# Kernel optimization log

Hardware: AMD Instinct MI355X
Metric: run time of the kernel (lower is better)

Reference implementation:

```python
import jax, jax.numpy as jnp
import numpy as np

C_Z = 128
C_H = 128
EPS = 1e-5


def _layer_norm(x, gamma, beta):
    mu = jnp.mean(x, axis=-1, keepdims=True)
    var = jnp.mean(jnp.square(x - mu), axis=-1, keepdims=True)
    return (x - mu) * jax.lax.rsqrt(var + EPS) * gamma + beta


def setup_inputs() -> dict:
    key = jax.random.key(0)
    ks = jax.random.split(key, 8)
    B, N = 1, 512
    s_z = 1.0 / np.sqrt(C_Z)
    s_h = 1.0 / np.sqrt(C_H)
    return {
        "z": jax.random.normal(ks[0], (B, N, N, C_Z), dtype=jnp.float32),
        "mask": jnp.ones((B, N, N), dtype=jnp.float32),
        # linear_ab_p: c_z -> 2*c_hidden
        "w_ab_p": jax.random.normal(ks[1], (2 * C_H, C_Z), dtype=jnp.float32) * s_z,
        "b_ab_p": jnp.zeros((2 * C_H,), dtype=jnp.float32),
        # linear_ab_g: c_z -> 2*c_hidden (gating init)
        "w_ab_g": jax.random.normal(ks[2], (2 * C_H, C_Z), dtype=jnp.float32) * s_z,
        "b_ab_g": jnp.ones((2 * C_H,), dtype=jnp.float32),
        # linear_g: c_z -> c_z (gating init)
        "w_g": jax.random.normal(ks[3], (C_Z, C_Z), dtype=jnp.float32) * s_z,
        "b_g": jnp.ones((C_Z,), dtype=jnp.float32),
        # linear_z: c_hidden -> c_z (final init)
        "w_z": jax.random.normal(ks[4], (C_Z, C_H), dtype=jnp.float32) * s_h,
        "b_z": jnp.zeros((C_Z,), dtype=jnp.float32),
        # layer norms
        "ln_in_g": jnp.ones((C_Z,), dtype=jnp.float32),
        "ln_in_b": jnp.zeros((C_Z,), dtype=jnp.float32),
        "ln_out_g": jnp.ones((C_H,), dtype=jnp.float32),
        "ln_out_b": jnp.zeros((C_H,), dtype=jnp.float32),
    }


def reference(z, mask, w_ab_p, b_ab_p, w_ab_g, b_ab_g, w_g, b_g, w_z, b_z,
              ln_in_g, ln_in_b, ln_out_g, ln_out_b):
    # [B, N, N, C] pair representation; outgoing triangle update
    zn = _layer_norm(z, ln_in_g, ln_in_b)
    m = mask[..., None]  # [B, N, N, 1]
    # gated dual projections: sigmoid(W_g z) * mask * (W_p z)  -> [B, N, N, 2H]
    gate = jax.nn.sigmoid(jnp.einsum("bijc,hc->bijh", zn, w_ab_g) + b_ab_g) * m
    ab = gate * (jnp.einsum("bijc,hc->bijh", zn, w_ab_p) + b_ab_p)
    a, b = jnp.split(ab, 2, axis=-1)  # each [B, N, N, H]
    # outgoing: x[b,i,j,h] = sum_k a[b,i,k,h] * b[b,j,k,h]
    x = jnp.einsum("bikh,bjkh->bijh", a, b)
    x = _layer_norm(x, ln_out_g, ln_out_b)
    out = (jnp.einsum("bijh,ch->bijc", x, w_z) + b_z)
    g = jax.nn.sigmoid(jnp.einsum("bijc,dc->bijd", zn, w_g) + b_g)
    return out * g
```

## Files before the change

kernel.cpp:

```cpp
#include <hip/hip_runtime.h>
#include <math.h>

#define NN 512
#define RR 262144
#define EPS_F 1e-5f

typedef unsigned short u16;
typedef unsigned int u32;
typedef __bf16 bf16x8 __attribute__((ext_vector_type(8)));
typedef float f32x4 __attribute__((ext_vector_type(4)));

__device__ __forceinline__ u16 f2bs(float f) {
  __bf16 h = (__bf16)f;
  return __builtin_bit_cast(u16, h);
}
__device__ __forceinline__ float bs2f(u16 u) {
  return (float)__builtin_bit_cast(__bf16, u);
}
__device__ __forceinline__ float sigmoidf_(float x) {
  return 1.f / (1.f + __expf(-x));
}

__global__ __launch_bounds__(256) void k_ln_in(const float* __restrict__ z,
                                               const float* __restrict__ g,
                                               const float* __restrict__ b,
                                               u16* __restrict__ zn) {
  const int w = threadIdx.x >> 6, l = threadIdx.x & 63;
  const long r = (long)blockIdx.x * 4 + w;
  const float2 v = *(const float2*)(z + r * 128 + l * 2);
  float s = v.x + v.y, sq = v.x * v.x + v.y * v.y;
#pragma unroll
  for (int m = 1; m < 64; m <<= 1) {
    s += __shfl_xor(s, m);
    sq += __shfl_xor(sq, m);
  }
  const float mu = s * 0.0078125f;
  const float var = sq * 0.0078125f - mu * mu;
  const float rs = rsqrtf(var + EPS_F);
  const float2 gg = *(const float2*)(g + l * 2);
  const float2 bb = *(const float2*)(b + l * 2);
  const u32 o = (u32)f2bs((v.x - mu) * rs * gg.x + bb.x) |
                ((u32)f2bs((v.y - mu) * rs * gg.y + bb.y) << 16);
  *(u32*)(zn + r * 128 + l * 2) = o;
}

__global__ __launch_bounds__(256) void k_proj(
    const u16* __restrict__ zn, const float* __restrict__ mask,
    const float* __restrict__ w_ab_p, const float* __restrict__ b_ab_p,
    const float* __restrict__ w_ab_g, const float* __restrict__ b_ab_g,
    const float* __restrict__ w_g, const float* __restrict__ b_g,
    u16* __restrict__ a_t, u16* __restrict__ b_t, u16* __restrict__ g_out) {
  __shared__ __align__(16) u16 As[128 * 136];
  __shared__ __align__(16) u16 Bs[128 * 136];
  __shared__ float maskS[128];
  const int t = threadIdx.x;
  const int tt = blockIdx.y;
  const long row0 = (long)blockIdx.x * 128;

  {
    const int row = t >> 1, half = t & 1;
    const uint4* src = (const uint4*)(zn + (row0 + row) * 128 + half * 64);
    uint4* dst = (uint4*)(As + row * 136 + half * 64);
#pragma unroll
    for (int i = 0; i < 8; ++i) dst[i] = src[i];
  }
  {
    const int n = t >> 1, half = t & 1;
    const float* src;
    if (tt < 4) {
      const int srow = tt * 64 + ((n >> 5) << 4) + (n & 15);
      src = (((n >> 4) & 1) ? w_ab_g : w_ab_p) + srow * 128 + half * 64;
    } else {
      src = w_g + n * 128 + half * 64;
    }
    u16* dst = Bs + n * 136 + half * 64;
#pragma unroll
    for (int i = 0; i < 16; ++i) {
      const float4 v = *(const float4*)(src + i * 4);
      dst[i * 4 + 0] = f2bs(v.x);
      dst[i * 4 + 1] = f2bs(v.y);
      dst[i * 4 + 2] = f2bs(v.z);
      dst[i * 4 + 3] = f2bs(v.w);
    }
  }
  if (t < 128) maskS[t] = mask[row0 + t];
  __syncthreads();

  const int lane = t & 63, wv = t >> 6;
  const int quad = lane >> 4, tl = lane & 15;
  const int wm = wv >> 1, wn = wv & 1;
  f32x4 acc[4][4];
#pragma unroll
  for (int mt = 0; mt < 4; ++mt)
#pragma unroll
    for (int nt = 0; nt < 4; ++nt) acc[mt][nt] = (f32x4){0.f, 0.f, 0.f, 0.f};

#pragma unroll
  for (int ks = 0; ks < 4; ++ks) {
    bf16x8 af[4], bfr[4];
#pragma unroll
    for (int mt = 0; mt < 4; ++mt)
      af[mt] = *(const bf16x8*)(As + (wm * 64 + mt * 16 + tl) * 136 + ks * 32 + quad * 8);
#pragma unroll
    for (int nt = 0; nt < 4; ++nt)
      bfr[nt] = *(const bf16x8*)(Bs + (wn * 64 + nt * 16 + tl) * 136 + ks * 32 + quad * 8);
#pragma unroll
    for (int mt = 0; mt < 4; ++mt)
#pragma unroll
      for (int nt = 0; nt < 4; ++nt)
        acc[mt][nt] = __builtin_amdgcn_mfma_f32_16x16x32_bf16(af[mt], bfr[nt], acc[mt][nt], 0, 0, 0);
  }

  if (tt < 4) {
    __syncthreads();
    u16* trans = As;
#pragma unroll
    for (int b2 = 0; b2 < 2; ++b2) {
      const int hl = wn * 32 + b2 * 16 + tl;
      const int hg = tt * 64 + hl;
      const float bp = b_ab_p[hg], bg = b_ab_g[hg];
#pragma unroll
      for (int mt = 0; mt < 4; ++mt) {
#pragma unroll
        for (int rg = 0; rg < 4; ++rg) {
          const int r = wm * 64 + mt * 16 + quad * 4 + rg;
          const float p = acc[mt][2 * b2][rg] + bp;
          const float gt = acc[mt][2 * b2 + 1][rg] + bg;
          trans[hl * 136 + r] = f2bs(sigmoidf_(gt) * maskS[r] * p);
        }
      }
    }
    __syncthreads();
    const int hl = t >> 2, qq = t & 3;
    const int hg = tt * 64 + hl;
    u16* dbuf = (tt < 2) ? a_t : b_t;
    const int hb = (tt < 2) ? hg : hg - 128;
    const uint4* src = (const uint4*)(trans + hl * 136 + qq * 32);
    uint4* dst = (uint4*)(dbuf + (long)hb * RR + row0 + qq * 32);
#pragma unroll
    for (int i = 0; i < 4; ++i) dst[i] = src[i];
  } else {
#pragma unroll
    for (int nt = 0; nt < 4; ++nt) {
      const int c = wn * 64 + nt * 16 + tl;
      const float bgc = b_g[c];
#pragma unroll
      for (int mt = 0; mt < 4; ++mt)
#pragma unroll
        for (int rg = 0; rg < 4; ++rg) {
          const int r = wm * 64 + mt * 16 + quad * 4 + rg;
          g_out[(row0 + r) * (long)128 + c] = f2bs(sigmoidf_(acc[mt][nt][rg] + bgc));
        }
    }
  }
}

__global__ __launch_bounds__(256) void k_tri(const u16* __restrict__ a_t,
                                             const u16* __restrict__ b_t,
                                             u16* __restrict__ x_t) {
  __shared__ __align__(16) u16 As[128 * 72];
  __shared__ __align__(16) u16 Bs[128 * 72];
  const int t = threadIdx.x;
  const int h = blockIdx.y;
  const int i0 = (blockIdx.x >> 2) * 128, j0 = (blockIdx.x & 3) * 128;
  const u16* Ag = a_t + (long)h * RR;
  const u16* Bg = b_t + (long)h * RR;
  const int lane = t & 63, wv = t >> 6;
  const int quad = lane >> 4, tl = lane & 15;
  const int wm = wv >> 1, wn = wv & 1;
  const int chunk = t & 7, rb = t >> 3;

  f32x4 acc[4][4];
#pragma unroll
  for (int mt = 0; mt < 4; ++mt)
#pragma unroll
    for (int nt = 0; nt < 4; ++nt) acc[mt][nt] = (f32x4){0.f, 0.f, 0.f, 0.f};

  for (int kt = 0; kt < 8; ++kt) {
    __syncthreads();
#pragma unroll
    for (int p = 0; p < 4; ++p) {
      const int row = rb + p * 32;
      *(uint4*)(As + row * 72 + chunk * 8) =
          *(const uint4*)(Ag + (long)(i0 + row) * 512 + kt * 64 + chunk * 8);
      *(uint4*)(Bs + row * 72 + chunk * 8) =
          *(const uint4*)(Bg + (long)(j0 + row) * 512 + kt * 64 + chunk * 8);
    }
    __syncthreads();
#pragma unroll
    for (int ks = 0; ks < 2; ++ks) {
      bf16x8 af[4], bfr[4];
#pragma unroll
      for (int mt = 0; mt < 4; ++mt)
        af[mt] = *(const bf16x8*)(As + (wm * 64 + mt * 16 + tl) * 72 + ks * 32 + quad * 8);
#pragma unroll
      for (int nt = 0; nt < 4; ++nt)
        bfr[nt] = *(const bf16x8*)(Bs + (wn * 64 + nt * 16 + tl) * 72 + ks * 32 + quad * 8);
#pragma unroll
      for (int mt = 0; mt < 4; ++mt)
#pragma unroll
        for (int nt = 0; nt < 4; ++nt)
          acc[mt][nt] = __builtin_amdgcn_mfma_f32_16x16x32_bf16(af[mt], bfr[nt], acc[mt][nt], 0, 0, 0);
    }
  }
#pragma unroll
  for (int mt = 0; mt < 4; ++mt)
#pragma unroll
    for (int nt = 0; nt < 4; ++nt)
#pragma unroll
      for (int rg = 0; rg < 4; ++rg) {
        const int i = i0 + wm * 64 + mt * 16 + quad * 4 + rg;
        const int j = j0 + wn * 64 + nt * 16 + tl;
        x_t[(long)h * RR + (long)i * 512 + j] = f2bs(acc[mt][nt][rg]);
      }
}

__global__ __launch_bounds__(256) void k_out(const u16* __restrict__ x_t,
                                             const float* __restrict__ w_z,
                                             const float* __restrict__ b_z,
                                             const float* __restrict__ ln_g,
                                             const float* __restrict__ ln_b,
                                             const u16* __restrict__ g_in,
                                             float* __restrict__ out) {
  __shared__ __align__(16) u16 Xs[128 * 136];
  __shared__ __align__(16) u16 Ws[128 * 136];
  __shared__ float lnGs[128], lnBs[128];
  const int t = threadIdx.x;
  const long row0 = (long)blockIdx.x * 128;

  if (t < 128) {
    lnGs[t] = ln_g[t];
    lnBs[t] = ln_b[t];
  }
  {
    const int hb = t >> 3, rq = t & 7;
    u32 xv[4][8];
#pragma unroll
    for (int hh = 0; hh < 4; ++hh) {
      const uint4* src = (const uint4*)(x_t + (long)(hb * 4 + hh) * RR + row0 + rq * 16);
      const uint4 a = src[0], b = src[1];
      xv[hh][0] = a.x; xv[hh][1] = a.y; xv[hh][2] = a.z; xv[hh][3] = a.w;
      xv[hh][4] = b.x; xv[hh][5] = b.y; xv[hh][6] = b.z; xv[hh][7] = b.w;
    }
#pragma unroll
    for (int rr = 0; rr < 16; ++rr) {
      const int wi = rr >> 1, sh = (rr & 1) * 16;
      const u32 e0 = (xv[0][wi] >> sh) & 0xffffu;
      const u32 e1 = (xv[1][wi] >> sh) & 0xffffu;
      const u32 e2 = (xv[2][wi] >> sh) & 0xffffu;
      const u32 e3 = (xv[3][wi] >> sh) & 0xffffu;
      *(uint2*)(Xs + (rq * 16 + rr) * 136 + hb * 4) = make_uint2(e0 | (e1 << 16), e2 | (e3 << 16));
    }
  }
  {
    const int n = t >> 1, half = t & 1;
    const float* src = w_z + n * 128 + half * 64;
    u16* dst = Ws + n * 136 + half * 64;
#pragma unroll
    for (int i = 0; i < 16; ++i) {
      const float4 v = *(const float4*)(src + i * 4);
      dst[i * 4 + 0] = f2bs(v.x);
      dst[i * 4 + 1] = f2bs(v.y);
      dst[i * 4 + 2] = f2bs(v.z);
      dst[i * 4 + 3] = f2bs(v.w);
    }
  }
  __syncthreads();
  {
    const int r = t >> 1, half = t & 1;
    u16* xr = Xs + r * 136 + half * 64;
    float vals[64];
    float s = 0.f, sq = 0.f;
#pragma unroll
    for (int i = 0; i < 64; ++i) {
      const float v = bs2f(xr[i]);
      vals[i] = v;
      s += v;
      sq += v * v;
    }
    s += __shfl_xor(s, 1);
    sq += __shfl_xor(sq, 1);
    const float mu = s * 0.0078125f;
    const float var = sq * 0.0078125f - mu * mu;
    const float rs = rsqrtf(var + EPS_F);
#pragma unroll
    for (int i = 0; i < 64; ++i) {
      const int hh = half * 64 + i;
      xr[i] = f2bs((vals[i] - mu) * rs * lnGs[hh] + lnBs[hh]);
    }
  }
  __syncthreads();

  const int lane = t & 63, wv = t >> 6;
  const int quad = lane >> 4, tl = lane & 15;
  const int wm = wv >> 1, wn = wv & 1;
  f32x4 acc[4][4];
#pragma unroll
  for (int mt = 0; mt < 4; ++mt)
#pragma unroll
    for (int nt = 0; nt < 4; ++nt) acc[mt][nt] = (f32x4){0.f, 0.f, 0.f, 0.f};

#pragma unroll
  for (int ks = 0; ks < 4; ++ks) {
    bf16x8 af[4], bfr[4];
#pragma unroll
    for (int mt = 0; mt < 4; ++mt)
      af[mt] = *(const bf16x8*)(Xs + (wm * 64 + mt * 16 + tl) * 136 + ks * 32 + quad * 8);
#pragma unroll
    for (int nt = 0; nt < 4; ++nt)
      bfr[nt] = *(const bf16x8*)(Ws + (wn * 64 + nt * 16 + tl) * 136 + ks * 32 + quad * 8);
#pragma unroll
    for (int mt = 0; mt < 4; ++mt)
#pragma unroll
      for (int nt = 0; nt < 4; ++nt)
        acc[mt][nt] = __builtin_amdgcn_mfma_f32_16x16x32_bf16(af[mt], bfr[nt], acc[mt][nt], 0, 0, 0);
  }
#pragma unroll
  for (int nt = 0; nt < 4; ++nt) {
    const int c = wn * 64 + nt * 16 + tl;
    const float bz = b_z[c];
#pragma unroll
    for (int mt = 0; mt < 4; ++mt)
#pragma unroll
      for (int rg = 0; rg < 4; ++rg) {
        const int r = wm * 64 + mt * 16 + quad * 4 + rg;
        const long idx = (row0 + r) * 128 + c;
        out[idx] = (acc[mt][nt][rg] + bz) * bs2f(g_in[idx]);
      }
  }
}

extern "C" void kernel_launch(void* const* d_in, const int* in_sizes, int n_in,
                              void* d_out, int out_size, void* d_ws, size_t ws_size,
                              hipStream_t stream) {
  const float* z = (const float*)d_in[0];
  const float* mask = (const float*)d_in[1];
  const float* w_ab_p = (const float*)d_in[2];
  const float* b_ab_p = (const float*)d_in[3];
  const float* w_ab_g = (const float*)d_in[4];
  const float* b_ab_g = (const float*)d_in[5];
  const float* w_g = (const float*)d_in[6];
  const float* b_g = (const float*)d_in[7];
  const float* w_z = (const float*)d_in[8];
  const float* b_z = (const float*)d_in[9];
  const float* ln_in_g = (const float*)d_in[10];
  const float* ln_in_b = (const float*)d_in[11];
  const float* ln_out_g = (const float*)d_in[12];
  const float* ln_out_b = (const float*)d_in[13];
  float* out = (float*)d_out;

  u16* zn = (u16*)d_ws;
  u16* a_t = zn + (size_t)RR * 128;
  u16* b_t = a_t + (size_t)RR * 128;
  u16* x_t = b_t + (size_t)RR * 128;
  u16* g_b = x_t + (size_t)RR * 128;

  k_ln_in<<<RR / 4, 256, 0, stream>>>(z, ln_in_g, ln_in_b, zn);
  k_proj<<<dim3(RR / 128, 5), 256, 0, stream>>>(zn, mask, w_ab_p, b_ab_p, w_ab_g,
                                                b_ab_g, w_g, b_g, a_t, b_t, g_b);
  k_tri<<<dim3(16, 128), 256, 0, stream>>>(a_t, b_t, x_t);
  k_out<<<RR / 128, 256, 0, stream>>>(x_t, w_z, b_z, ln_out_g, ln_out_b, g_b, out);
}
```

Before: 580.4 us.

## Fuse input layernorm into projection kernel and pre-convert weights once

Removes the standalone input layer-norm kernel and the bf16 normalized-z intermediate. The projection kernel now reads fp32 z directly, normalizes each row in registers and writes bf16 into shared memory. Each block then loops over all five weight tiles instead of launching five blocks per row tile, so z is read and normalized only once. A small prepass converts all weights to bf16 in the permuted layout, which removes per-block fp32-to-bf16 weight conversion. The cost is fewer, longer blocks with more register pressure (64-float arrays) and serialized weight tiles within each block.

```diff
diff --git a/kernel.cpp b/kernel.cpp
--- a/kernel.cpp
+++ b/kernel.cpp
@@ -21,136 +21,153 @@
   return 1.f / (1.f + __expf(-x));
 }
 
-__global__ __launch_bounds__(256) void k_ln_in(const float* __restrict__ z,
-                                               const float* __restrict__ g,
-                                               const float* __restrict__ b,
-                                               u16* __restrict__ zn) {
-  const int w = threadIdx.x >> 6, l = threadIdx.x & 63;
-  const long r = (long)blockIdx.x * 4 + w;
-  const float2 v = *(const float2*)(z + r * 128 + l * 2);
-  float s = v.x + v.y, sq = v.x * v.x + v.y * v.y;
-#pragma unroll
-  for (int m = 1; m < 64; m <<= 1) {
-    s += __shfl_xor(s, m);
-    sq += __shfl_xor(sq, m);
-  }
-  const float mu = s * 0.0078125f;
-  const float var = sq * 0.0078125f - mu * mu;
-  const float rs = rsqrtf(var + EPS_F);
-  const float2 gg = *(const float2*)(g + l * 2);
-  const float2 bb = *(const float2*)(b + l * 2);
-  const u32 o = (u32)f2bs((v.x - mu) * rs * gg.x + bb.x) |
-                ((u32)f2bs((v.y - mu) * rs * gg.y + bb.y) << 16);
-  *(u32*)(zn + r * 128 + l * 2) = o;
+__global__ __launch_bounds__(256) void k_wconv(const float* __restrict__ w_ab_p,
+                                               const float* __restrict__ w_ab_g,
+                                               const float* __restrict__ w_g,
+                                               u16* __restrict__ wb) {
+  const int u = blockIdx.x * 256 + threadIdx.x;
+  const int row = u >> 5;
+  const int c4 = (u & 31) * 4;
+  const float* src;
+  if (row < 512) {
+    const int tt = row >> 7, n = row & 127;
+    const int srow = tt * 64 + ((n >> 5) << 4) + (n & 15);
+    src = (((n >> 4) & 1) ? w_ab_g : w_ab_p) + srow * 128 + c4;
+  } else {
+    src = w_g + (row - 512) * 128 + c4;
+  }
+  const float4 v = *(const float4*)src;
+  u16 o[4] = {f2bs(v.x), f2bs(v.y), f2bs(v.z), f2bs(v.w)};
+  *(uint2*)(wb + row * 128 + c4) = *(uint2*)o;
 }
 
 __global__ __launch_bounds__(256) void k_proj(
-    const u16* __restrict__ zn, const float* __restrict__ mask,
-    const float* __restrict__ w_ab_p, const float* __restrict__ b_ab_p,
-    const float* __restrict__ w_ab_g, const float* __restrict__ b_ab_g,
-    const float* __restrict__ w_g, const float* __restrict__ b_g,
+    const float* __restrict__ z, const float* __restrict__ mask,
+    const u16* __restrict__ wb, const float* __restrict__ b_ab_p,
+    const float* __restrict__ b_ab_g, const float* __restrict__ b_g,
+    const float* __restrict__ ln_g, const float* __restrict__ ln_b,
     u16* __restrict__ a_t, u16* __restrict__ b_t, u16* __restrict__ g_out) {
   __shared__ __align__(16) u16 As[128 * 136];
   __shared__ __align__(16) u16 Bs[128 * 136];
   __shared__ float maskS[128];
   const int t = threadIdx.x;
-  const int tt = blockIdx.y;
   const long row0 = (long)blockIdx.x * 128;
 
   {
     const int row = t >> 1, half = t & 1;
-    const uint4* src = (const uint4*)(zn + (row0 + row) * 128 + half * 64);
+    const float* zr = z + (row0 + row) * 128 + half * 64;
+    float vals[64];
+    float s = 0.f, sq = 0.f;
+#pragma unroll
+    for (int i = 0; i < 16; ++i) {
+      const float4 v = *(const float4*)(zr + i * 4);
+      vals[i * 4 + 0] = v.x;
+      vals[i * 4 + 1] = v.y;
+      vals[i * 4 + 2] = v.z;
+      vals[i * 4 + 3] = v.w;
+      s += v.x + v.y + v.z + v.w;
+      sq += v.x * v.x + v.y * v.y + v.z * v.z + v.w * v.w;
+    }
+    s += __shfl_xor(s, 1);
+    sq += __shfl_xor(sq, 1);
+    const float mu = s * 0.0078125f;
+    const float var = sq * 0.0078125f - mu * mu;
+    const float rs = rsqrtf(var + EPS_F);
+    u16 ob[64];
+#pragma unroll
+    for (int i = 0; i < 16; ++i) {
+      const float4 gg = *(const float4*)(ln_g + half * 64 + i * 4);
+      const float4 bb = *(const float4*)(ln_b + half * 64 + i * 4);
+      ob[i * 4 + 0] = f2bs((vals[i * 4 + 0] - mu) * rs * gg.x + bb.x);
+      ob[i * 4 + 1] = f2bs((vals[i * 4 + 1] - mu) * rs * gg.y + bb.y);
+      ob[i * 4 + 2] = f2bs((vals[i * 4 + 2] - mu) * rs * gg.z + bb.z);
+      ob[i * 4 + 3] = f2bs((vals[i * 4 + 3] - mu) * rs * gg.w + bb.w);
+    }
     uint4* dst = (uint4*)(As + row * 136 + half * 64);
-#pragma unroll
-    for (int i = 0; i < 8; ++i) dst[i] = src[i];
-  }
-  {
-    const int n = t >> 1, half = t & 1;
-    const float* src;
-    if (tt < 4) {
-      const int srow = tt * 64 + ((n >> 5) << 4) + (n & 15);
-      src = (((n >> 4) & 1) ? w_ab_g : w_ab_p) + srow * 128 + half * 64;
-    } else {
-      src = w_g + n * 128 + half * 64;
-    }
-    u16* dst = Bs + n * 136 + half * 64;
-#pragma unroll
-    for (int i = 0; i < 16; ++i) {
-      const float4 v = *(const float4*)(src + i * 4);
-      dst[i * 4 + 0] = f2bs(v.x);
-      dst[i * 4 + 1] = f2bs(v.y);
-      dst[i * 4 + 2] = f2bs(v.z);
-      dst[i * 4 + 3] = f2bs(v.w);
-    }
+    const uint4* sp = (const uint4*)ob;
+#pragma unroll
+    for (int i = 0; i < 8; ++i) dst[i] = sp[i];
   }
   if (t < 128) maskS[t] = mask[row0 + t];
-  __syncthreads();
 
   const int lane = t & 63, wv = t >> 6;
   const int quad = lane >> 4, tl = lane & 15;
   const int wm = wv >> 1, wn = wv & 1;
-  f32x4 acc[4][4];
-#pragma unroll
-  for (int mt = 0; mt < 4; ++mt)
-#pragma unroll
-    for (int nt = 0; nt < 4; ++nt) acc[mt][nt] = (f32x4){0.f, 0.f, 0.f, 0.f};
-
-#pragma unroll
-  for (int ks = 0; ks < 4; ++ks) {
-    bf16x8 af[4], bfr[4];
+
+  for (int tt = 0; tt < 5; ++tt) {
+    {
+      const int n = t >> 1, half = t & 1;
+      const uint4* src = (const uint4*)(wb + (tt * 128 + n) * 128 + half * 64);
+      uint4* dst = (uint4*)(Bs + n * 136 + half * 64);
+#pragma unroll
+      for (int i = 0; i < 8; ++i) dst[i] = src[i];
+    }
+    __syncthreads();
+
+    f32x4 acc[4][4];
 #pragma unroll
     for (int mt = 0; mt < 4; ++mt)
-      af[mt] = *(const bf16x8*)(As + (wm * 64 + mt * 16 + tl) * 136 + ks * 32 + quad * 8);
-#pragma unroll
-    for (int nt = 0; nt < 4; ++nt)
-      bfr[nt] = *(const bf16x8*)(Bs + (wn * 64 + nt * 16 + tl) * 136 + ks * 32 + quad * 8);
-#pragma unroll
-    for (int mt = 0; mt < 4; ++mt)
+#pragma unroll
+      for (int nt = 0; nt < 4; ++nt) acc[mt][nt] = (f32x4){0.f, 0.f, 0.f, 0.f};
+
+#pragma unroll
+    for (int ks = 0; ks < 4; ++ks) {
+      bf16x8 af[4], bfr[4];
+#pragma unroll
+      for (int mt = 0; mt < 4; ++mt)
+        af[mt] = *(const bf16x8*)(As + (wm * 64 + mt * 16 + tl) * 136 + ks * 32 + quad * 8);
 #pragma unroll
       for (int nt = 0; nt < 4; ++nt)
-        acc[mt][nt] = __builtin_amdgcn_mfma_f32_16x16x32_bf16(af[mt], bfr[nt], acc[mt][nt], 0, 0, 0);
-  }
-
-  if (tt < 4) {
+        bfr[nt] = *(const bf16x8*)(Bs + (wn * 64 + nt * 16 + tl) * 136 + ks * 32 + quad * 8);
+#pragma unroll
+      for (int mt = 0; mt < 4; ++mt)
+#pragma unroll
+        for (int nt = 0; nt < 4; ++nt)
+          acc[mt][nt] = __builtin_amdgcn_mfma_f32_16x16x32_bf16(af[mt], bfr[nt], acc[mt][nt], 0, 0, 0);
+    }
     __syncthreads();
-    u16* trans = As;
-#pragma unroll
-    for (int b2 = 0; b2 < 2; ++b2) {
-      const int hl = wn * 32 + b2 * 16 + tl;
-      const int hg = tt * 64 + hl;
-      const float bp = b_ab_p[hg], bg = b_ab_g[hg];
-#pragma unroll
-      for (int mt = 0; mt < 4; ++mt) {
-#pragma unroll
-        for (int rg = 0; rg < 4; ++rg) {
-          const int r = wm * 64 + mt * 16 + quad * 4 + rg;
-          const float p = acc[mt][2 * b2][rg] + bp;
-          const float gt = acc[mt][2 * b2 + 1][rg] + bg;
-          trans[hl * 136 + r] = f2bs(sigmoidf_(gt) * maskS[r] * p);
-        }
-      }
-    }
-    __syncthreads();
-    const int hl = t >> 2, qq = t & 3;
-    const int hg = tt * 64 + hl;
-    u16* dbuf = (tt < 2) ? a_t : b_t;
-    const int hb = (tt < 2) ? hg : hg - 128;
-    const uint4* src = (const uint4*)(trans + hl * 136 + qq * 32);
-    uint4* dst = (uint4*)(dbuf + (long)hb * RR + row0 + qq * 32);
-#pragma unroll
-    for (int i = 0; i < 4; ++i) dst[i] = src[i];
-  } else {
-#pragma unroll
-    for (int nt = 0; nt < 4; ++nt) {
-      const int c = wn * 64 + nt * 16 + tl;
-      const float bgc = b_g[c];
-#pragma unroll
-      for (int mt = 0; mt < 4; ++mt)
-#pragma unroll
-        for (int rg = 0; rg < 4; ++rg) {
-          const int r = wm * 64 + mt * 16 + quad * 4 + rg;
-          g_out[(row0 + r) * (long)128 + c] = f2bs(sigmoidf_(acc[mt][nt][rg] + bgc));
-        }
+
+    if (tt < 4) {
+#pragma unroll
+      for (int b2 = 0; b2 < 2; ++b2) {
+        const int hl = wn * 32 + b2 * 16 + tl;
+        const int hg = tt * 64 + hl;
+        const float bp = b_ab_p[hg], bg = b_ab_g[hg];
+#pragma unroll
+        for (int mt = 0; mt < 4; ++mt)
+#pragma unroll
+          for (int rg = 0; rg < 4; ++rg) {
+            const int r = wm * 64 + mt * 16 + quad * 4 + rg;
+            const float p = acc[mt][2 * b2][rg] + bp;
+            const float gt = acc[mt][2 * b2 + 1][rg] + bg;
+            Bs[hl * 136 + r] = f2bs(sigmoidf_(gt) * maskS[r] * p);
+          }
+      }
+      __syncthreads();
+      {
+        const int hl = t >> 2, qq = t & 3;
+        const int hg = tt * 64 + hl;
+        u16* dbuf = (tt < 2) ? a_t : b_t;
+        const int hb = (tt < 2) ? hg : hg - 128;
+        const uint4* src = (const uint4*)(Bs + hl * 136 + qq * 32);
+        uint4* dst = (uint4*)(dbuf + (long)hb * RR + row0 + qq * 32);
+#pragma unroll
+        for (int i = 0; i < 4; ++i) dst[i] = src[i];
+      }
+      __syncthreads();
+    } else {
+#pragma unroll
+      for (int nt = 0; nt < 4; ++nt) {
+        const int c = wn * 64 + nt * 16 + tl;
+        const float bgc = b_g[c];
+#pragma unroll
+        for (int mt = 0; mt < 4; ++mt)
+#pragma unroll
+          for (int rg = 0; rg < 4; ++rg) {
+            const int r = wm * 64 + mt * 16 + quad * 4 + rg;
+            g_out[(row0 + r) * (long)128 + c] = f2bs(sigmoidf_(acc[mt][nt][rg] + bgc));
+          }
+      }
     }
   }
 }
@@ -349,15 +366,15 @@
   const float* ln_out_b = (const float*)d_in[13];
   float* out = (float*)d_out;
 
-  u16* zn = (u16*)d_ws;
-  u16* a_t = zn + (size_t)RR * 128;
+  u16* a_t = (u16*)d_ws;
   u16* b_t = a_t + (size_t)RR * 128;
   u16* x_t = b_t + (size_t)RR * 128;
   u16* g_b = x_t + (size_t)RR * 128;
-
-  k_ln_in<<<RR / 4, 256, 0, stream>>>(z, ln_in_g, ln_in_b, zn);
-  k_proj<<<dim3(RR / 128, 5), 256, 0, stream>>>(zn, mask, w_ab_p, b_ab_p, w_ab_g,
-                                                b_ab_g, w_g, b_g, a_t, b_t, g_b);
+  u16* wb = g_b + (size_t)RR * 128;
+
+  k_wconv<<<80, 256, 0, stream>>>(w_ab_p, w_ab_g, w_g, wb);
+  k_proj<<<RR / 128, 256, 0, stream>>>(z, mask, wb, b_ab_p, b_ab_g, b_g,
+                                       ln_in_g, ln_in_b, a_t, b_t, g_b);
   k_tri<<<dim3(16, 128), 256, 0, stream>>>(a_t, b_t, x_t);
   k_out<<<RR / 128, 256, 0, stream>>>(x_t, w_z, b_z, ln_out_g, ln_out_b, g_b, out);
 }
```

Result: no change. 577.7 us (-0.5%).
